# Kernel tuning notes

Hardware: AMD Instinct MI355X
Metric: run time of the kernel (lower is better)

The kernel has to match this reference:

```python
import jax, jax.numpy as jnp
import numpy as np

B, L, D = 64, 4096, 512

def setup_inputs() -> dict:
    key = jax.random.key(0)
    k1, k2 = jax.random.split(key)
    current_hidden = jax.random.normal(k1, (B, D), dtype=jnp.float32)
    encoder_outputs = jax.random.normal(k2, (B, L, D), dtype=jnp.float32)
    return {"current_hidden": current_hidden, "encoder_outputs": encoder_outputs}

def reference(current_hidden, encoder_outputs):
    # energy[b, l] = <current_hidden[b], encoder_outputs[b, l]>  (fused batched matmul,
    # replacing the per-timestep python loop of tiny bmms)
    energy = jnp.einsum('bd,bld->bl', current_hidden, encoder_outputs)
    # softmax over the source-length axis (nn.Softmax(dim=1))
    alignment = jax.nn.softmax(energy, axis=1)  # [B, L]
    # context = mean over L of alignment[..., None] * encoder_outputs
    # (original uses torch.mean, i.e. weighted sum divided by L)
    L_ = encoder_outputs.shape[1]
    context = jnp.einsum('bl,bld->bd', alignment, encoder_outputs) / L_
    return context
```

## Files before the change

### kernel.cpp

```cpp
#include <hip/hip_runtime.h>


#define D_DIM 512
#define B_DIM 64
#define L_DIM 4096
#define C_CHUNK 32
#define WPB 4
#define WAVES_PER_B (C_CHUNK * WPB)
#define ROWS_PER_WAVE (L_DIM / WAVES_PER_B)

__global__ __launch_bounds__(256, 8) void attn_pass1i(
    const float* __restrict__ h,
    const float* __restrict__ enc,
    float* __restrict__ part_ms,
    float* __restrict__ part_ctx)
{
    const int b    = blockIdx.y;
    const int c    = blockIdx.x;
    const int tid  = threadIdx.x;
    const int wave = tid >> 6;
    const int lane = tid & 63;
    const int g    = c * WPB + wave;

    const float4* h4 = reinterpret_cast<const float4*>(h + (size_t)b * D_DIM);
    const float4 h0 = h4[lane];
    const float4 h1 = h4[lane + 64];

    const float* rowp = enc + ((size_t)b * L_DIM + (size_t)g) * D_DIM + 4 * lane;
    const size_t rowStride = (size_t)WAVES_PER_B * D_DIM;

    float m = -3.0e38f;
    float s = 0.0f;
    float4 a0 = {0.f, 0.f, 0.f, 0.f};
    float4 a1 = {0.f, 0.f, 0.f, 0.f};

    float4 v0 = *reinterpret_cast<const float4*>(rowp);
    float4 v1 = *reinterpret_cast<const float4*>(rowp + 256);

    for (int r = 0; r < ROWS_PER_WAVE; ++r) {
        const float* np = rowp + ((r + 1 < ROWS_PER_WAVE) ? rowStride : 0);
        const float4 nv0 = *reinterpret_cast<const float4*>(np);
        const float4 nv1 = *reinterpret_cast<const float4*>(np + 256);

        float e = h0.x * v0.x + h0.y * v0.y + h0.z * v0.z + h0.w * v0.w
                + h1.x * v1.x + h1.y * v1.y + h1.z * v1.z + h1.w * v1.w;
        #pragma unroll
        for (int off = 32; off > 0; off >>= 1)
            e += __shfl_xor(e, off, 64);
        if (e > m) {
            const float alpha = __expf(m - e);
            s *= alpha;
            a0.x *= alpha; a0.y *= alpha; a0.z *= alpha; a0.w *= alpha;
            a1.x *= alpha; a1.y *= alpha; a1.z *= alpha; a1.w *= alpha;
            m = e;
        }
        const float w = __expf(e - m);
        s += w;
        a0.x += w * v0.x; a0.y += w * v0.y; a0.z += w * v0.z; a0.w += w * v0.w;
        a1.x += w * v1.x; a1.y += w * v1.y; a1.z += w * v1.z; a1.w += w * v1.w;

        v0 = nv0; v1 = nv1;
        rowp += rowStride;
    }

    __shared__ float sm_m[4];
    __shared__ float sm_s[4];
    __shared__ float sm_ctx[4][D_DIM];

    reinterpret_cast<float4*>(&sm_ctx[wave][0])[lane]   = a0;
    reinterpret_cast<float4*>(&sm_ctx[wave][256])[lane] = a1;
    if (lane == 0) { sm_m[wave] = m; sm_s[wave] = s; }
    __syncthreads();

    const float M  = fmaxf(fmaxf(sm_m[0], sm_m[1]), fmaxf(sm_m[2], sm_m[3]));
    const float w0 = __expf(sm_m[0] - M);
    const float w1 = __expf(sm_m[1] - M);
    const float w2 = __expf(sm_m[2] - M);
    const float w3 = __expf(sm_m[3] - M);

    if (tid == 0) {
        const float S = sm_s[0] * w0 + sm_s[1] * w1 + sm_s[2] * w2 + sm_s[3] * w3;
        float* ms = part_ms + ((size_t)b * C_CHUNK + c) * 2;
        ms[0] = M;
        ms[1] = S;
    }

    float* dst = part_ctx + ((size_t)b * C_CHUNK + c) * D_DIM;
    for (int d = tid; d < D_DIM; d += 256) {
        dst[d] = sm_ctx[0][d] * w0 + sm_ctx[1][d] * w1
               + sm_ctx[2][d] * w2 + sm_ctx[3][d] * w3;
    }
}

__global__ __launch_bounds__(256) void attn_pass2(
    const float* __restrict__ part_ms,
    const float* __restrict__ part_ctx,
    float* __restrict__ out,
    float invL)
{
    const int b   = blockIdx.x;
    const int tid = threadIdx.x;

    __shared__ float w_sm[C_CHUNK];
    __shared__ float invSL;

    if (tid == 0) {
        const float* ms = part_ms + (size_t)b * C_CHUNK * 2;
        float M = -3.0e38f;
        for (int i = 0; i < C_CHUNK; ++i) M = fmaxf(M, ms[2 * i]);
        float S = 0.f;
        for (int i = 0; i < C_CHUNK; ++i) {
            const float w = __expf(ms[2 * i] - M);
            w_sm[i] = w;
            S += w * ms[2 * i + 1];
        }
        invSL = invL / S;
    }
    __syncthreads();

    const float scale = invSL;
    for (int d = tid; d < D_DIM; d += 256) {
        float acc = 0.f;
        #pragma unroll 8
        for (int i = 0; i < C_CHUNK; ++i)
            acc += w_sm[i] * part_ctx[((size_t)b * C_CHUNK + i) * D_DIM + d];
        out[(size_t)b * D_DIM + d] = acc * scale;
    }
}

extern "C" void kernel_launch(void* const* d_in, const int* in_sizes, int n_in,
                              void* d_out, int out_size, void* d_ws, size_t ws_size,
                              hipStream_t stream) {
    const float* h   = (const float*)d_in[0];
    const float* enc = (const float*)d_in[1];
    float* out = (float*)d_out;

    float* part_ms  = (float*)d_ws;
    float* part_ctx = part_ms + (size_t)B_DIM * C_CHUNK * 2;

    dim3 grid1(C_CHUNK, B_DIM);
    attn_pass1i<<<grid1, 256, 0, stream>>>(h, enc, part_ms, part_ctx);
    attn_pass2<<<B_DIM, 256, 0, stream>>>(part_ms, part_ctx, out,
                                          1.0f / (float)L_DIM);
}
```

Baseline: 689.8 us.

## Process encoder rows in double-buffered groups of four per wave

Restructures the main pass so each wave loads four contiguous rows at a time into double-buffered registers and processes one group while the next is in flight. The four shuffle reductions are interleaved and the online-softmax rescale is done once per group. The chunk count is halved so each wave covers a contiguous range. The goal is more outstanding memory requests per wave to hide HBM latency, at the cost of higher register use and fewer blocks.

```diff
diff --git a/kernel.cpp b/kernel.cpp
--- a/kernel.cpp
+++ b/kernel.cpp
@@ -4,12 +4,69 @@
 #define D_DIM 512
 #define B_DIM 64
 #define L_DIM 4096
-#define C_CHUNK 32
+#define C_CHUNK 16
 #define WPB 4
-#define WAVES_PER_B (C_CHUNK * WPB)
-#define ROWS_PER_WAVE (L_DIM / WAVES_PER_B)
+#define ROWS_PER_WAVE (L_DIM / (C_CHUNK * WPB))
+#define GRP 4
+#define NGRP (ROWS_PER_WAVE / GRP)
 
-__global__ __launch_bounds__(256, 8) void attn_pass1i(
+struct Row { float4 lo, hi; };
+
+__device__ __forceinline__ float dot8(const float4 h0, const float4 h1,
+                                      const float4 v0, const float4 v1) {
+    return h0.x * v0.x + h0.y * v0.y + h0.z * v0.z + h0.w * v0.w
+         + h1.x * v1.x + h1.y * v1.y + h1.z * v1.z + h1.w * v1.w;
+}
+
+__device__ __forceinline__ void load_group(Row (&buf)[GRP], const float* p) {
+    #pragma unroll
+    for (int i = 0; i < GRP; ++i) {
+        buf[i].lo = *reinterpret_cast<const float4*>(p + i * D_DIM);
+        buf[i].hi = *reinterpret_cast<const float4*>(p + i * D_DIM + 256);
+    }
+}
+
+__device__ __forceinline__ void process_group(
+    const Row (&buf)[GRP], const float4 h0, const float4 h1,
+    float& m, float& s, float4& a0, float4& a1)
+{
+    float e[GRP];
+    #pragma unroll
+    for (int i = 0; i < GRP; ++i)
+        e[i] = dot8(h0, h1, buf[i].lo, buf[i].hi);
+
+    #pragma unroll
+    for (int off = 32; off > 0; off >>= 1) {
+        #pragma unroll
+        for (int i = 0; i < GRP; ++i)
+            e[i] += __shfl_xor(e[i], off, 64);
+    }
+
+    const float gm = fmaxf(fmaxf(e[0], e[1]), fmaxf(e[2], e[3]));
+    if (gm > m) {
+        const float alpha = __expf(m - gm);
+        s *= alpha;
+        a0.x *= alpha; a0.y *= alpha; a0.z *= alpha; a0.w *= alpha;
+        a1.x *= alpha; a1.y *= alpha; a1.z *= alpha; a1.w *= alpha;
+        m = gm;
+    }
+
+    float w[GRP];
+    float ws = 0.f;
+    #pragma unroll
+    for (int i = 0; i < GRP; ++i) { w[i] = __expf(e[i] - m); ws += w[i]; }
+    s += ws;
+
+    #pragma unroll
+    for (int i = 0; i < GRP; ++i) {
+        a0.x += w[i] * buf[i].lo.x; a0.y += w[i] * buf[i].lo.y;
+        a0.z += w[i] * buf[i].lo.z; a0.w += w[i] * buf[i].lo.w;
+        a1.x += w[i] * buf[i].hi.x; a1.y += w[i] * buf[i].hi.y;
+        a1.z += w[i] * buf[i].hi.z; a1.w += w[i] * buf[i].hi.w;
+    }
+}
+
+__global__ __launch_bounds__(256, 4) void attn_pass1g(
     const float* __restrict__ h,
     const float* __restrict__ enc,
     float* __restrict__ part_ms,
@@ -20,48 +77,33 @@
     const int tid  = threadIdx.x;
     const int wave = tid >> 6;
     const int lane = tid & 63;
-    const int g    = c * WPB + wave;
+
+    const int l0 = c * (L_DIM / C_CHUNK) + wave * ROWS_PER_WAVE;
 
     const float4* h4 = reinterpret_cast<const float4*>(h + (size_t)b * D_DIM);
     const float4 h0 = h4[lane];
     const float4 h1 = h4[lane + 64];
 
-    const float* rowp = enc + ((size_t)b * L_DIM + (size_t)g) * D_DIM + 4 * lane;
-    const size_t rowStride = (size_t)WAVES_PER_B * D_DIM;
+    const float* base = enc + ((size_t)b * L_DIM + (size_t)l0) * D_DIM + 4 * lane;
+    const size_t gstride = (size_t)GRP * D_DIM;
 
     float m = -3.0e38f;
     float s = 0.0f;
     float4 a0 = {0.f, 0.f, 0.f, 0.f};
     float4 a1 = {0.f, 0.f, 0.f, 0.f};
 
-    float4 v0 = *reinterpret_cast<const float4*>(rowp);
-    float4 v1 = *reinterpret_cast<const float4*>(rowp + 256);
+    Row bufA[GRP], bufB[GRP];
+    load_group(bufA, base);
 
-    for (int r = 0; r < ROWS_PER_WAVE; ++r) {
-        const float* np = rowp + ((r + 1 < ROWS_PER_WAVE) ? rowStride : 0);
-        const float4 nv0 = *reinterpret_cast<const float4*>(np);
-        const float4 nv1 = *reinterpret_cast<const float4*>(np + 256);
-
-        float e = h0.x * v0.x + h0.y * v0.y + h0.z * v0.z + h0.w * v0.w
-                + h1.x * v1.x + h1.y * v1.y + h1.z * v1.z + h1.w * v1.w;
-        #pragma unroll
-        for (int off = 32; off > 0; off >>= 1)
-            e += __shfl_xor(e, off, 64);
-        if (e > m) {
-            const float alpha = __expf(m - e);
-            s *= alpha;
-            a0.x *= alpha; a0.y *= alpha; a0.z *= alpha; a0.w *= alpha;
-            a1.x *= alpha; a1.y *= alpha; a1.z *= alpha; a1.w *= alpha;
-            m = e;
-        }
-        const float w = __expf(e - m);
-        s += w;
-        a0.x += w * v0.x; a0.y += w * v0.y; a0.z += w * v0.z; a0.w += w * v0.w;
-        a1.x += w * v1.x; a1.y += w * v1.y; a1.z += w * v1.z; a1.w += w * v1.w;
-
-        v0 = nv0; v1 = nv1;
-        rowp += rowStride;
+    for (int g = 0; g < NGRP - 2; g += 2) {
+        load_group(bufB, base + (size_t)(g + 1) * gstride);
+        process_group(bufA, h0, h1, m, s, a0, a1);
+        load_group(bufA, base + (size_t)(g + 2) * gstride);
+        process_group(bufB, h0, h1, m, s, a0, a1);
     }
+    load_group(bufB, base + (size_t)(NGRP - 1) * gstride);
+    process_group(bufA, h0, h1, m, s, a0, a1);
+    process_group(bufB, h0, h1, m, s, a0, a1);
 
     __shared__ float sm_m[4];
     __shared__ float sm_s[4];
@@ -121,7 +163,7 @@
     const float scale = invSL;
     for (int d = tid; d < D_DIM; d += 256) {
         float acc = 0.f;
-        #pragma unroll 8
+        #pragma unroll
         for (int i = 0; i < C_CHUNK; ++i)
             acc += w_sm[i] * part_ctx[((size_t)b * C_CHUNK + i) * D_DIM + d];
         out[(size_t)b * D_DIM + d] = acc * scale;
@@ -139,7 +181,7 @@
     float* part_ctx = part_ms + (size_t)B_DIM * C_CHUNK * 2;
 
     dim3 grid1(C_CHUNK, B_DIM);
-    attn_pass1i<<<grid1, 256, 0, stream>>>(h, enc, part_ms, part_ctx);
+    attn_pass1g<<<grid1, 256, 0, stream>>>(h, enc, part_ms, part_ctx);
     attn_pass2<<<B_DIM, 256, 0, stream>>>(part_ms, part_ctx, out,
                                           1.0f / (float)L_DIM);
 }
```

After: 677.7 us. No clear change (-1.7%).
